# Performance work log

Hardware: AMD Instinct MI355X
Metric: run time of the kernel (lower is better)

Reference implementation:

```python
import jax, jax.numpy as jnp
import numpy as np

N_NODES = 100000
N_EDGES = 1600000
IN_DIM = 128
HEADS = 4
HID = 32            # per-head channels; HEADS*HID == 128 == IN_DIM
HC = HEADS * HID
NUM_CLASSES = 349
NUM_LAYERS = 2
BN_EPS = 1e-5
NEG_SLOPE = 0.2     # PyG GATConv default leaky_relu slope


def _gat_conv(x, src, dst, Wsrc, Wdst, a_src, a_dst, bias):
    """PyG GATConv (concat=True). x:[N,F] -> [N,H*C]."""
    N = x.shape[0]
    xs = (x @ Wsrc).reshape(N, HEADS, HID)   # source-side projection
    xd = (x @ Wdst).reshape(N, HEADS, HID)   # dest-side projection
    s_src = jnp.einsum('nhc,hc->nh', xs, a_src)   # [N,H]
    s_dst = jnp.einsum('nhc,hc->nh', xd, a_dst)   # [N,H]
    e = jax.nn.leaky_relu(s_src[src] + s_dst[dst], NEG_SLOPE)   # [E,H]
    # numerically-stable edge softmax grouped by destination node
    m = jax.ops.segment_max(e, dst, num_segments=N)             # [N,H]
    m = jnp.where(jnp.isfinite(m), m, 0.0)                      # isolated nodes
    p = jnp.exp(e - m[dst])                                     # [E,H]
    denom = jax.ops.segment_sum(p, dst, num_segments=N)         # [N,H]
    alpha = p / (denom[dst] + 1e-16)                            # [E,H]
    msg = xs[src] * alpha[:, :, None]                           # [E,H,C]
    out = jax.ops.segment_sum(msg, dst, num_segments=N)         # [N,H,C]
    return out.reshape(N, HC) + bias


def _batch_norm(x, gamma, beta):
    mu = x.mean(0)
    var = x.var(0)
    return gamma * (x - mu) * jax.lax.rsqrt(var + BN_EPS) + beta


def setup_inputs() -> dict:
    key = jax.random.key(0)
    ks = jax.random.split(key, 8)
    sc = 1.0 / np.sqrt(IN_DIM)
    inp = {
        'x': jax.random.normal(ks[0], (N_NODES, IN_DIM), jnp.float32),
        'edge_index': jax.random.randint(ks[1], (2, N_EDGES), 0, N_NODES, jnp.int32),
        'W_src': jax.random.normal(ks[2], (NUM_LAYERS, IN_DIM, HC), jnp.float32) * sc,
        'W_dst': jax.random.normal(ks[3], (NUM_LAYERS, IN_DIM, HC), jnp.float32) * sc,
        'att_src': jax.random.normal(ks[4], (NUM_LAYERS, HEADS, HID), jnp.float32) * sc,
        'att_dst': jax.random.normal(ks[5], (NUM_LAYERS, HEADS, HID), jnp.float32) * sc,
        'conv_bias': jnp.zeros((NUM_LAYERS, HC), jnp.float32),
        'lin_W': jax.random.normal(ks[6], (NUM_LAYERS, IN_DIM, HC), jnp.float32) * sc,
        'lin_b': jnp.zeros((NUM_LAYERS, HC), jnp.float32),
        'bn_gamma': jnp.ones((NUM_LAYERS, HC), jnp.float32),
        'bn_beta': jnp.zeros((NUM_LAYERS, HC), jnp.float32),
        'fc_W': jax.random.normal(ks[7], (IN_DIM, NUM_CLASSES), jnp.float32) * sc,
        'fc_b': jnp.zeros((NUM_CLASSES,), jnp.float32),
    }
    return inp


def reference(x, edge_index, W_src, W_dst, att_src, att_dst, conv_bias,
              lin_W, lin_b, bn_gamma, bn_beta, fc_W, fc_b):
    src, dst = edge_index[0], edge_index[1]
    for i in range(NUM_LAYERS):
        h = _gat_conv(x, src, dst, W_src[i], W_dst[i], att_src[i], att_dst[i],
                      conv_bias[i])
        h = h + x @ lin_W[i] + lin_b[i]          # skip projection
        h = _batch_norm(h, bn_gamma[i], bn_beta[i])
        x = jax.nn.relu(h)                        # dropout p=0.2 omitted (eval)
    return x @ fc_W + fc_b
```

## Files before the change

### kernel.cpp

```cpp
#include <hip/hip_runtime.h>
#include <hip/hip_bf16.h>
#include <stdint.h>

#define N_NODES 100000
#define N_EDGES 1600000
#define IN_DIM 128
#define HEADS 4
#define HID 32
#define HC 128
#define NUM_CLASSES 349
#define NUM_LAYERS 2
#define BN_EPS 1e-5f
#define NEG_SLOPE 0.2f
#define NCAT 264
#define MP 100032

#define NPARAM 144861

#define NBKT 782
#define ECHUNK 8192
#define NCHUNK ((N_EDGES + ECHUNK - 1) / ECHUNK)
#define NTOT (NBKT * NCHUNK)
#define SCAN_CHUNK 1024
#define SCAN2_BLOCKS ((NTOT + SCAN_CHUNK - 1) / SCAN_CHUNK)

using bf16 = __hip_bfloat16;
typedef __attribute__((ext_vector_type(8))) short short8;
typedef __attribute__((ext_vector_type(4))) float floatx4;

__device__ __forceinline__ float b2f(bf16 v) { return __bfloat162float(v); }

__global__ void detect_dtype(const uint32_t* __restrict__ xw, int* __restrict__ flag) {
    int lane = threadIdx.x;
    int insane = 0;
    for (int i = lane; i < 256; i += 64) {
        uint32_t lo = xw[i] & 0xffffu;
        uint32_t e = (lo >> 7) & 0xffu;
        if (lo != 0u && (e < 100u || e > 150u)) insane++;
    }
    for (int off = 32; off > 0; off >>= 1) insane += __shfl_down(insane, off, 64);
    if (lane == 0) *flag = (insane > 64) ? 1 : 0;
}

__global__ void cvt_params(const void* p0, const void* p1, const void* p2, const void* p3,
                           const void* p4, const void* p5, const void* p6, const void* p7,
                           const void* p8, const void* p9, const void* p10,
                           float* __restrict__ out, const int* __restrict__ flag) {
    int i = blockIdx.x * blockDim.x + threadIdx.x;
    if (i >= NPARAM) return;
    bool isf32 = (*flag != 0);
    const void* p; int off;
    if      (i < 32768)  { p = p0;  off = i; }
    else if (i < 65536)  { p = p1;  off = i - 32768; }
    else if (i < 65792)  { p = p2;  off = i - 65536; }
    else if (i < 66048)  { p = p3;  off = i - 65792; }
    else if (i < 66304)  { p = p4;  off = i - 66048; }
    else if (i < 99072)  { p = p5;  off = i - 66304; }
    else if (i < 99328)  { p = p6;  off = i - 99072; }
    else if (i < 99584)  { p = p7;  off = i - 99328; }
    else if (i < 99840)  { p = p8;  off = i - 99584; }
    else if (i < 144512) { p = p9;  off = i - 99840; }
    else                 { p = p10; off = i - 144512; }
    out[i] = isf32 ? ((const float*)p)[off] : b2f(((const bf16*)p)[off]);
}

__global__ void pack_bcat(const float* __restrict__ Wsrc, const float* __restrict__ Wdst,
                          const float* __restrict__ asrc, const float* __restrict__ adst,
                          const float* __restrict__ linW, bf16* __restrict__ Bp) {
    int idx = blockIdx.x * blockDim.x + threadIdx.x;
    if (idx >= 17 * 2048) return;
    int j = idx & 7, lane = (idx >> 3) & 63, kt = (idx >> 9) & 3, nt = idx >> 11;
    int n = nt * 16 + (lane & 15);
    int k = kt * 32 + ((lane >> 4) << 3) + j;
    float v = 0.f;
    if (n < 128) {
        v = Wsrc[k * HC + n];
    } else if (n < 132) {
        int h = n - 128;
        for (int c = 0; c < HID; c++) v += Wsrc[k * HC + h * HID + c] * asrc[h * HID + c];
    } else if (n < 136) {
        int h = n - 132;
        for (int c = 0; c < HID; c++) v += Wdst[k * HC + h * HID + c] * adst[h * HID + c];
    } else if (n < 264) {
        v = linW[k * HC + (n - 136)];
    }
    Bp[idx] = __float2bfloat16(v);
}

__global__ void pack_b(const float* __restrict__ src, int ld, int nvalid,
                       bf16* __restrict__ Bp, int total) {
    int idx = blockIdx.x * blockDim.x + threadIdx.x;
    if (idx >= total) return;
    int j = idx & 7, lane = (idx >> 3) & 63, kt = (idx >> 9) & 3, nt = idx >> 11;
    int n = nt * 16 + (lane & 15);
    int k = kt * 32 + ((lane >> 4) << 3) + j;
    float v = (n < nvalid) ? src[k * ld + n] : 0.f;
    Bp[idx] = __float2bfloat16(v);
}

template <int MODE>
__global__ __launch_bounds__(256) void gemm_mfma_proj(
    const void* __restrict__ Araw, const int* __restrict__ flag,
    const bf16* __restrict__ Bp,
    bf16* __restrict__ xs, bf16* __restrict__ scA, bf16* __restrict__ xlin,
    const float* __restrict__ gamma, const float* __restrict__ beta,
    const float* __restrict__ bnsum, const float* __restrict__ bnsq) {
    __shared__ bf16 As[64 * 128];
    int tid = threadIdx.x;
    size_t rowbase = (size_t)blockIdx.x * 64;
    int4* la = (int4*)As;
    const float invN = 1.f / (float)N_NODES;
    if (MODE == 0) {
        bool isf32 = (*flag != 0);
#pragma unroll
        for (int s = 0; s < 4; s++) {
            int idx = s * 256 + tid;
            size_t grow = rowbase + (idx >> 4);
            int cg = idx & 15;
            int4 outv = {0, 0, 0, 0};
            if (grow < N_NODES) {
                if (isf32) {
                    const float* xr = (const float*)Araw + grow * 128 + cg * 8;
                    float4 f0 = ((const float4*)xr)[0];
                    float4 f1 = ((const float4*)xr)[1];
                    bf16* ov = (bf16*)&outv;
                    ov[0] = __float2bfloat16(f0.x); ov[1] = __float2bfloat16(f0.y);
                    ov[2] = __float2bfloat16(f0.z); ov[3] = __float2bfloat16(f0.w);
                    ov[4] = __float2bfloat16(f1.x); ov[5] = __float2bfloat16(f1.y);
                    ov[6] = __float2bfloat16(f1.z); ov[7] = __float2bfloat16(f1.w);
                } else {
                    outv = ((const int4*)Araw)[grow * 16 + cg];
                }
            }
            la[idx] = outv;
        }
    } else {
        const bf16* A = (const bf16*)Araw;
        const int4* ga = (const int4*)(A + rowbase * 128);
#pragma unroll
        for (int s = 0; s < 4; s++) {
            int4 raw = ga[s * 256 + tid];
            bf16* hv = (bf16*)&raw;
            int cbase = ((s * 256 + tid) & 15) * 8;
            int4 outv; bf16* ov = (bf16*)&outv;
#pragma unroll
            for (int j = 0; j < 8; j++) {
                int c = cbase + j;
                float mu = bnsum[c] * invN;
                float var = bnsq[c] * invN - mu * mu;
                float v = gamma[c] * (b2f(hv[j]) - mu) * rsqrtf(var + BN_EPS) + beta[c];
                ov[j] = __float2bfloat16(v > 0.f ? v : 0.f);
            }
            la[s * 256 + tid] = outv;
        }
    }
    __syncthreads();
    int wave = tid >> 6, lane = tid & 63;
    int arow = wave * 16 + (lane & 15);
    int acol = (lane >> 4) * 8;
    short8 afrag[4];
#pragma unroll
    for (int kt = 0; kt < 4; kt++)
        afrag[kt] = *(const short8*)&As[arow * 128 + kt * 32 + acol];
    const short8* bbase = (const short8*)Bp + lane;
    int colb = lane & 15;
    int row0 = wave * 16 + (lane >> 4) * 4;
#pragma unroll
    for (int nt = 0; nt < 17; nt++) {
        floatx4 acc = {0.f, 0.f, 0.f, 0.f};
#pragma unroll
        for (int kt = 0; kt < 4; kt++)
            acc = __builtin_amdgcn_mfma_f32_16x16x32_bf16(afrag[kt], bbase[(nt * 4 + kt) * 64], acc, 0, 0, 0);
        int col = nt * 16 + colb;
#pragma unroll
        for (int r = 0; r < 4; r++) {
            size_t row = rowbase + row0 + r;
            bf16 v = __float2bfloat16(acc[r]);
            if (col < 128)       xs[row * HC + col] = v;
            else if (col < 136)  scA[row * 8 + (col - 128)] = v;
            else { int q = col - 136; if (q < 128) xlin[row * HC + q] = v; }
        }
    }
}

__global__ __launch_bounds__(256) void gemm_mfma_out(
    const bf16* __restrict__ A, const bf16* __restrict__ Bp,
    const float* __restrict__ bias,
    const float* __restrict__ gamma, const float* __restrict__ beta,
    const float* __restrict__ bnsum, const float* __restrict__ bnsq,
    void* __restrict__ C, const int* __restrict__ flag) {
    __shared__ bf16 As[64 * 128];
    int tid = threadIdx.x;
    size_t rowbase = (size_t)blockIdx.x * 64;
    const int4* ga = (const int4*)(A + rowbase * 128);
    int4* la = (int4*)As;
    const float invN = 1.f / (float)N_NODES;
#pragma unroll
    for (int s = 0; s < 4; s++) {
        int4 raw = ga[s * 256 + tid];
        bf16* hv = (bf16*)&raw;
        int cbase = ((s * 256 + tid) & 15) * 8;
        int4 outv; bf16* ov = (bf16*)&outv;
#pragma unroll
        for (int j = 0; j < 8; j++) {
            int c = cbase + j;
            float mu = bnsum[c] * invN;
            float var = bnsq[c] * invN - mu * mu;
            float v = gamma[c] * (b2f(hv[j]) - mu) * rsqrtf(var + BN_EPS) + beta[c];
            ov[j] = __float2bfloat16(v > 0.f ? v : 0.f);
        }
        la[s * 256 + tid] = outv;
    }
    __syncthreads();
    int wave = tid >> 6, lane = tid & 63;
    int arow = wave * 16 + (lane & 15);
    int acol = (lane >> 4) * 8;
    short8 afrag[4];
#pragma unroll
    for (int kt = 0; kt < 4; kt++)
        afrag[kt] = *(const short8*)&As[arow * 128 + kt * 32 + acol];
    const short8* bbase = (const short8*)Bp + lane;
    int colb = lane & 15;
    int row0 = wave * 16 + (lane >> 4) * 4;
    bool isf32 = (*flag != 0);
    for (int nt = 0; nt < 22; nt++) {
        floatx4 acc = {0.f, 0.f, 0.f, 0.f};
#pragma unroll
        for (int kt = 0; kt < 4; kt++)
            acc = __builtin_amdgcn_mfma_f32_16x16x32_bf16(afrag[kt], bbase[(nt * 4 + kt) * 64], acc, 0, 0, 0);
        int col = nt * 16 + colb;
        if (col >= NUM_CLASSES) continue;
        float bv = bias[col];
#pragma unroll
        for (int r = 0; r < 4; r++) {
            size_t row = rowbase + row0 + r;
            if (row < N_NODES) {
                float v = acc[r] + bv;
                if (isf32) ((float*)C)[row * NUM_CLASSES + col] = v;
                else       ((bf16*)C)[row * NUM_CLASSES + col] = __float2bfloat16(v);
            }
        }
    }
}

__global__ __launch_bounds__(256) void bucket_hist(const int* __restrict__ dst,
                                                   int* __restrict__ cnt) {
    __shared__ int h[NBKT];
    int t = threadIdx.x;
    for (int i = t; i < NBKT; i += 256) h[i] = 0;
    __syncthreads();
    int base = blockIdx.x * ECHUNK;
    int end = base + ECHUNK; if (end > N_EDGES) end = N_EDGES;
    for (int i = base + t; i < end; i += 256)
        atomicAdd(&h[dst[i] >> 7], 1);
    __syncthreads();
    for (int i = t; i < NBKT; i += 256)
        cnt[i * NCHUNK + blockIdx.x] = h[i];
}

__global__ void scan_partial(const int* __restrict__ counts, int* __restrict__ bsum, int n) {
    __shared__ int red[256];
    int t = threadIdx.x;
    int base = blockIdx.x * SCAN_CHUNK + t * 4;
    int s = 0;
#pragma unroll
    for (int j = 0; j < 4; j++) {
        int idx = base + j;
        if (idx < n) s += counts[idx];
    }
    red[t] = s;
    __syncthreads();
    for (int off = 128; off > 0; off >>= 1) {
        if (t < off) red[t] += red[t + off];
        __syncthreads();
    }
    if (t == 0) bsum[blockIdx.x] = red[0];
}

__global__ void scan_final(int* __restrict__ counts, const int* __restrict__ bsum, int n) {
    __shared__ int ts[256];
    __shared__ int pre[256];
    int t = threadIdx.x;
    int pv = (t < (int)blockIdx.x) ? bsum[t] : 0;
    pre[t] = pv;
    int base = blockIdx.x * SCAN_CHUNK + t * 4;
    int c[4];
    int mysum = 0;
#pragma unroll
    for (int j = 0; j < 4; j++) {
        int idx = base + j;
        c[j] = (idx < n) ? counts[idx] : 0;
        mysum += c[j];
    }
    ts[t] = mysum;
    __syncthreads();
    for (int off = 128; off > 0; off >>= 1) {
        if (t < off) pre[t] += pre[t + off];
        __syncthreads();
    }
    for (int off = 1; off < 256; off <<= 1) {
        int v = (t >= off) ? ts[t - off] : 0;
        __syncthreads();
        ts[t] += v;
        __syncthreads();
    }
    int run = pre[0] + ts[t] - mysum;
#pragma unroll
    for (int j = 0; j < 4; j++) {
        int idx = base + j;
        if (idx < n) {
            counts[idx] = run;
            run += c[j];
        }
    }
}

__global__ __launch_bounds__(256) void bucket_scatter(const int* __restrict__ src,
                                                      const int* __restrict__ dst,
                                                      const int* __restrict__ cntscan,
                                                      uint32_t* __restrict__ sorted) {
    __shared__ int cur[NBKT];
    int t = threadIdx.x;
    for (int i = t; i < NBKT; i += 256)
        cur[i] = cntscan[i * NCHUNK + blockIdx.x];
    __syncthreads();
    int base = blockIdx.x * ECHUNK;
    int end = base + ECHUNK; if (end > N_EDGES) end = N_EDGES;
    for (int i = base + t; i < end; i += 256) {
        int d = dst[i];
        int b = d >> 7;
        int pos = atomicAdd(&cur[b], 1);
        sorted[pos] = ((uint32_t)(d & 127) << 17) | (uint32_t)src[i];
    }
}

__global__ __launch_bounds__(256) void bucket_csr(const uint32_t* __restrict__ sorted,
                                                  const int* __restrict__ cntscan,
                                                  int* __restrict__ srcs,
                                                  int* __restrict__ offsets) {
    __shared__ int cnt128[128];
    __shared__ int sc[128];
    __shared__ int cur[128];
    int b = blockIdx.x, t = threadIdx.x;
    int ebeg = cntscan[b * NCHUNK];
    int eend = (b == NBKT - 1) ? N_EDGES : cntscan[(b + 1) * NCHUNK];
    if (t < 128) cnt128[t] = 0;
    __syncthreads();
    uint32_t buf[10];
    int k = 0;
    for (int e = ebeg + t; e < eend; e += 256) {
        uint32_t u = sorted[e];
        if (k < 10) buf[k] = u;
        k++;
        atomicAdd(&cnt128[u >> 17], 1);
    }
    __syncthreads();
    if (t < 128) sc[t] = cnt128[t];
    __syncthreads();
    for (int off = 1; off < 128; off <<= 1) {
        int v = 0;
        if (t < 128 && t >= off) v = sc[t - off];
        __syncthreads();
        if (t < 128) sc[t] += v;
        __syncthreads();
    }
    if (t < 128) {
        int node = b * 128 + t;
        if (node < N_NODES) offsets[node] = ebeg + sc[t];
        cur[t] = ebeg + sc[t] - cnt128[t];
    }
    __syncthreads();
    int k2 = 0;
    for (int e = ebeg + t; e < eend; e += 256) {
        uint32_t u = (k2 < 10) ? buf[k2] : sorted[e];
        k2++;
        int ld = (int)(u >> 17);
        int pos = atomicAdd(&cur[ld], 1);
        srcs[pos] = (int)(u & 0x1FFFFu);
    }
}

__device__ __forceinline__ void edge_acc(int s, int h, int c0, float s_dst,
                                         const bf16* __restrict__ xs,
                                         const bf16* __restrict__ scA,
                                         float& den, float& n0, float& n1) {
    float sc = b2f(scA[(size_t)s * 8 + h]) + s_dst;
    sc = sc > 0.f ? sc : NEG_SLOPE * sc;
    float e = __expf(sc);
    __hip_bfloat162 xv = *reinterpret_cast<const __hip_bfloat162*>(&xs[(size_t)s * HC + c0]);
    den += e;
    n0 += b2f(xv.x) * e;
    n1 += b2f(xv.y) * e;
}

__global__ __launch_bounds__(256) void gat_gather(
    const int* __restrict__ srcs, const int* __restrict__ offsets,
    const bf16* __restrict__ xs, const bf16* __restrict__ scA,
    const bf16* __restrict__ xlin,
    const float* __restrict__ cbias, const float* __restrict__ lbias,
    bf16* __restrict__ hout) {
    int n = blockIdx.x * 4 + (threadIdx.x >> 6);
    int lane = threadIdx.x & 63;
    int c0 = lane * 2;
    int h = c0 >> 5;
    int beg = (n == 0) ? 0 : offsets[n - 1];
    int end = offsets[n];
    float s_dst = b2f(scA[(size_t)n * 8 + 4 + h]);
    float den = 0.f, n0 = 0.f, n1 = 0.f;
    int i = beg;
    for (; i + 7 < end; i += 8) {
        int s0 = srcs[i],     s1 = srcs[i + 1], s2 = srcs[i + 2], s3 = srcs[i + 3];
        int s4 = srcs[i + 4], s5 = srcs[i + 5], s6 = srcs[i + 6], s7 = srcs[i + 7];
        edge_acc(s0, h, c0, s_dst, xs, scA, den, n0, n1);
        edge_acc(s1, h, c0, s_dst, xs, scA, den, n0, n1);
        edge_acc(s2, h, c0, s_dst, xs, scA, den, n0, n1);
        edge_acc(s3, h, c0, s_dst, xs, scA, den, n0, n1);
        edge_acc(s4, h, c0, s_dst, xs, scA, den, n0, n1);
        edge_acc(s5, h, c0, s_dst, xs, scA, den, n0, n1);
        edge_acc(s6, h, c0, s_dst, xs, scA, den, n0, n1);
        edge_acc(s7, h, c0, s_dst, xs, scA, den, n0, n1);
    }
    for (; i + 3 < end; i += 4) {
        int s0 = srcs[i], s1 = srcs[i + 1], s2 = srcs[i + 2], s3 = srcs[i + 3];
        edge_acc(s0, h, c0, s_dst, xs, scA, den, n0, n1);
        edge_acc(s1, h, c0, s_dst, xs, scA, den, n0, n1);
        edge_acc(s2, h, c0, s_dst, xs, scA, den, n0, n1);
        edge_acc(s3, h, c0, s_dst, xs, scA, den, n0, n1);
    }
    for (; i < end; i++)
        edge_acc(srcs[i], h, c0, s_dst, xs, scA, den, n0, n1);
    float r = 1.f / (den + 1e-16f);
    __hip_bfloat162 xl = *reinterpret_cast<const __hip_bfloat162*>(&xlin[(size_t)n * HC + c0]);
    float v0 = n0 * r + b2f(xl.x) + cbias[c0] + lbias[c0];
    float v1 = n1 * r + b2f(xl.y) + cbias[c0 + 1] + lbias[c0 + 1];
    __hip_bfloat162 hv;
    hv.x = __float2bfloat16(v0);
    hv.y = __float2bfloat16(v1);
    *reinterpret_cast<__hip_bfloat162*>(&hout[(size_t)n * HC + c0]) = hv;
}

__global__ void bn_stats(const bf16* __restrict__ h, float* __restrict__ bnsum,
                         float* __restrict__ bnsq) {
    int c = threadIdx.x & 127;
    int half = threadIdx.x >> 7;
    int r0 = blockIdx.x * 500;
    int rend = r0 + 500; if (rend > N_NODES) rend = N_NODES;
    float s1 = 0.f, s2 = 0.f;
    for (int r = r0 + half; r < rend; r += 2) {
        float v = b2f(h[(size_t)r * HC + c]);
        s1 += v; s2 += v * v;
    }
    atomicAdd(&bnsum[c], s1);
    atomicAdd(&bnsq[c], s2);
}

extern "C" void kernel_launch(void* const* d_in, const int* in_sizes, int n_in,
                              void* d_out, int out_size, void* d_ws, size_t ws_size,
                              hipStream_t stream) {
    const void* x_in = d_in[0];
    const int*  edge = (const int*)d_in[1];
    const int* esrc = edge;
    const int* edst = edge + N_EDGES;

    bf16* xbh  = (bf16*)d_ws;
    bf16* xs   = xbh + (size_t)MP * HC;
    bf16* scA  = xs + (size_t)MP * HC;
    bf16* xlin = scA + (size_t)MP * 8;
    bf16* Bp   = xlin + (size_t)MP * HC;
    bf16* fcWp = Bp + 17 * 2048;
    float* bnstat = (float*)(fcWp + 22 * 2048);
    int*   flag  = (int*)(bnstat + 512);
    int*   bsum  = flag + 4;
    float* parms = (float*)(bsum + SCAN2_BLOCKS + 2);
    float* Wsrc_f  = parms;
    float* Wdst_f  = parms + 32768;
    float* asrc_f  = parms + 65536;
    float* adst_f  = parms + 65792;
    float* cbias_f = parms + 66048;
    float* linW_f  = parms + 66304;
    float* linb_f  = parms + 99072;
    float* gamma_f = parms + 99328;
    float* beta_f  = parms + 99584;
    float* fcW_f   = parms + 99840;
    float* fcb_f   = parms + 144512;

    int* srcs    = (int*)d_out;
    int* offsets = srcs + N_EDGES;
    uint32_t* sorted = (uint32_t*)(offsets + N_NODES);
    int* cnt = (int*)(sorted + N_EDGES);

    detect_dtype<<<1, 64, 0, stream>>>((const uint32_t*)x_in, flag);

    cvt_params<<<(NPARAM + 255) / 256, 256, 0, stream>>>(
        d_in[2], d_in[3], d_in[4], d_in[5], d_in[6], d_in[7], d_in[8],
        d_in[9], d_in[10], d_in[11], d_in[12], parms, flag);

    bucket_hist<<<NCHUNK, 256, 0, stream>>>(edst, cnt);
    scan_partial<<<SCAN2_BLOCKS, 256, 0, stream>>>(cnt, bsum, NTOT);
    scan_final<<<SCAN2_BLOCKS, 256, 0, stream>>>(cnt, bsum, NTOT);
    bucket_scatter<<<NCHUNK, 256, 0, stream>>>(esrc, edst, cnt, sorted);
    bucket_csr<<<NBKT, 256, 0, stream>>>(sorted, cnt, srcs, offsets);

    pack_b<<<(22 * 2048 + 255) / 256, 256, 0, stream>>>(fcW_f, NUM_CLASSES, NUM_CLASSES,
                                                        fcWp, 22 * 2048);
    hipMemsetAsync(bnstat, 0, 512 * sizeof(float), stream);

    for (int layer = 0; layer < NUM_LAYERS; layer++) {
        const int woff = layer * IN_DIM * HC;
        const int aoff = layer * HEADS * HID;
        const int boff = layer * HC;
        float* bns = bnstat + layer * 256;
        float* bnq = bns + 128;

        pack_bcat<<<(17 * 2048 + 255) / 256, 256, 0, stream>>>(
            Wsrc_f + woff, Wdst_f + woff, asrc_f + aoff, adst_f + aoff,
            linW_f + woff, Bp);

        if (layer == 0) {
            gemm_mfma_proj<0><<<MP / 64, 256, 0, stream>>>(
                x_in, flag, Bp, xs, scA, xlin, nullptr, nullptr, nullptr, nullptr);
        } else {
            float* pbns = bnstat + (layer - 1) * 256;
            gemm_mfma_proj<1><<<MP / 64, 256, 0, stream>>>(
                xbh, nullptr, Bp, xs, scA, xlin,
                gamma_f + (layer - 1) * HC, beta_f + (layer - 1) * HC,
                pbns, pbns + 128);
        }

        gat_gather<<<N_NODES / 4, 256, 0, stream>>>(
            srcs, offsets, xs, scA, xlin, cbias_f + boff, linb_f + boff, xbh);

        bn_stats<<<200, 256, 0, stream>>>(xbh, bns, bnq);
    }

    gemm_mfma_out<<<MP / 64, 256, 0, stream>>>(
        xbh, fcWp, fcb_f, gamma_f + HC, beta_f + HC,
        bnstat + 256, bnstat + 256 + 128, d_out, flag);
}
```

Before: 703.1 us.

## Fuse CSR build into cooperative kernel, merge packs, restructure GEMM B reuse

Folds the five-kernel bucket-sort CSR build (histogram, two scans, scatter, per-bucket CSR) into one cooperative kernel that uses grid syncs. It also merges the weight-packing kernels into a single launch and moves the BN-stat zeroing into detect_dtype, so fewer kernels are launched. The GEMMs now keep B fragments in registers per wave and loop over row tiles, and BN scale/shift is precomputed once per block in shared memory. The gather loop prefetches the next batch of source indices. The cooperative launch needs all 391 blocks resident at once, and the larger register footprint may lower occupancy.

```diff
diff --git a/kernel.cpp b/kernel.cpp
--- a/kernel.cpp
+++ b/kernel.cpp
@@ -1,6 +1,9 @@
 #include <hip/hip_runtime.h>
 #include <hip/hip_bf16.h>
+#include <hip/hip_cooperative_groups.h>
 #include <stdint.h>
+
+namespace cg = cooperative_groups;
 
 #define N_NODES 100000
 #define N_EDGES 1600000
@@ -12,17 +15,22 @@
 #define NUM_LAYERS 2
 #define BN_EPS 1e-5f
 #define NEG_SLOPE 0.2f
-#define NCAT 264
 #define MP 100032
 
 #define NPARAM 144861
 
 #define NBKT 782
-#define ECHUNK 8192
-#define NCHUNK ((N_EDGES + ECHUNK - 1) / ECHUNK)
+#define ECHUNK 4096
+#define NCHUNK 391
 #define NTOT (NBKT * NCHUNK)
-#define SCAN_CHUNK 1024
-#define SCAN2_BLOCKS ((NTOT + SCAN_CHUNK - 1) / SCAN_CHUNK)
+#define SCAN_CHUNK 2048
+#define SCANB ((NTOT + SCAN_CHUNK - 1) / SCAN_CHUNK)
+
+#define BP_NT 20
+#define FC_NT 24
+#define BP_ELEMS (BP_NT * 2048)
+#define FC_ELEMS (FC_NT * 2048)
+#define PACK_TOTAL (2 * BP_ELEMS + FC_ELEMS)
 
 using bf16 = __hip_bfloat16;
 typedef __attribute__((ext_vector_type(8))) short short8;
@@ -30,8 +38,10 @@
 
 __device__ __forceinline__ float b2f(bf16 v) { return __bfloat162float(v); }
 
-__global__ void detect_dtype(const uint32_t* __restrict__ xw, int* __restrict__ flag) {
+__global__ void detect_dtype(const uint32_t* __restrict__ xw, int* __restrict__ flag,
+                             float* __restrict__ bnstat) {
     int lane = threadIdx.x;
+    for (int i = lane; i < 512; i += 64) bnstat[i] = 0.f;
     int insane = 0;
     for (int i = lane; i < 256; i += 64) {
         uint32_t lo = xw[i] & 0xffffu;
@@ -64,38 +74,45 @@
     out[i] = isf32 ? ((const float*)p)[off] : b2f(((const bf16*)p)[off]);
 }
 
-__global__ void pack_bcat(const float* __restrict__ Wsrc, const float* __restrict__ Wdst,
-                          const float* __restrict__ asrc, const float* __restrict__ adst,
-                          const float* __restrict__ linW, bf16* __restrict__ Bp) {
-    int idx = blockIdx.x * blockDim.x + threadIdx.x;
-    if (idx >= 17 * 2048) return;
-    int j = idx & 7, lane = (idx >> 3) & 63, kt = (idx >> 9) & 3, nt = idx >> 11;
-    int n = nt * 16 + (lane & 15);
-    int k = kt * 32 + ((lane >> 4) << 3) + j;
-    float v = 0.f;
-    if (n < 128) {
-        v = Wsrc[k * HC + n];
-    } else if (n < 132) {
-        int h = n - 128;
-        for (int c = 0; c < HID; c++) v += Wsrc[k * HC + h * HID + c] * asrc[h * HID + c];
-    } else if (n < 136) {
-        int h = n - 132;
-        for (int c = 0; c < HID; c++) v += Wdst[k * HC + h * HID + c] * adst[h * HID + c];
-    } else if (n < 264) {
-        v = linW[k * HC + (n - 136)];
-    }
-    Bp[idx] = __float2bfloat16(v);
-}
-
-__global__ void pack_b(const float* __restrict__ src, int ld, int nvalid,
-                       bf16* __restrict__ Bp, int total) {
-    int idx = blockIdx.x * blockDim.x + threadIdx.x;
-    if (idx >= total) return;
-    int j = idx & 7, lane = (idx >> 3) & 63, kt = (idx >> 9) & 3, nt = idx >> 11;
-    int n = nt * 16 + (lane & 15);
-    int k = kt * 32 + ((lane >> 4) << 3) + j;
-    float v = (n < nvalid) ? src[k * ld + n] : 0.f;
-    Bp[idx] = __float2bfloat16(v);
+__global__ void pack_all(const float* __restrict__ Wsrc0, const float* __restrict__ Wdst0,
+                         const float* __restrict__ asrc0, const float* __restrict__ adst0,
+                         const float* __restrict__ linW0, const float* __restrict__ fcW,
+                         bf16* __restrict__ Bp0, bf16* __restrict__ Bp1,
+                         bf16* __restrict__ fcWp) {
+    int gid = blockIdx.x * blockDim.x + threadIdx.x;
+    if (gid >= PACK_TOTAL) return;
+    if (gid < 2 * BP_ELEMS) {
+        int layer = gid / BP_ELEMS;
+        int idx = gid - layer * BP_ELEMS;
+        const float* Wsrc = Wsrc0 + layer * IN_DIM * HC;
+        const float* Wdst = Wdst0 + layer * IN_DIM * HC;
+        const float* asrc = asrc0 + layer * HEADS * HID;
+        const float* adst = adst0 + layer * HEADS * HID;
+        const float* linW = linW0 + layer * IN_DIM * HC;
+        int j = idx & 7, lane = (idx >> 3) & 63, kt = (idx >> 9) & 3, nt = idx >> 11;
+        int n = nt * 16 + (lane & 15);
+        int k = kt * 32 + ((lane >> 4) << 3) + j;
+        float v = 0.f;
+        if (n < 128) {
+            v = Wsrc[k * HC + n];
+        } else if (n < 132) {
+            int h = n - 128;
+            for (int c = 0; c < HID; c++) v += Wsrc[k * HC + h * HID + c] * asrc[h * HID + c];
+        } else if (n < 136) {
+            int h = n - 132;
+            for (int c = 0; c < HID; c++) v += Wdst[k * HC + h * HID + c] * adst[h * HID + c];
+        } else if (n < 264) {
+            v = linW[k * HC + (n - 136)];
+        }
+        (layer == 0 ? Bp0 : Bp1)[idx] = __float2bfloat16(v);
+    } else {
+        int idx = gid - 2 * BP_ELEMS;
+        int j = idx & 7, lane = (idx >> 3) & 63, kt = (idx >> 9) & 3, nt = idx >> 11;
+        int n = nt * 16 + (lane & 15);
+        int k = kt * 32 + ((lane >> 4) << 3) + j;
+        float v = (n < NUM_CLASSES) ? fcW[k * NUM_CLASSES + n] : 0.f;
+        fcWp[idx] = __float2bfloat16(v);
+    }
 }
 
 template <int MODE>
@@ -106,21 +123,21 @@
     const float* __restrict__ gamma, const float* __restrict__ beta,
     const float* __restrict__ bnsum, const float* __restrict__ bnsq) {
     __shared__ bf16 As[64 * 128];
+    __shared__ float sc_s[128], sh_s[128];
     int tid = threadIdx.x;
     size_t rowbase = (size_t)blockIdx.x * 64;
     int4* la = (int4*)As;
-    const float invN = 1.f / (float)N_NODES;
     if (MODE == 0) {
         bool isf32 = (*flag != 0);
 #pragma unroll
         for (int s = 0; s < 4; s++) {
             int idx = s * 256 + tid;
             size_t grow = rowbase + (idx >> 4);
-            int cg = idx & 15;
+            int cg16 = idx & 15;
             int4 outv = {0, 0, 0, 0};
             if (grow < N_NODES) {
                 if (isf32) {
-                    const float* xr = (const float*)Araw + grow * 128 + cg * 8;
+                    const float* xr = (const float*)Araw + grow * 128 + cg16 * 8;
                     float4 f0 = ((const float4*)xr)[0];
                     float4 f1 = ((const float4*)xr)[1];
                     bf16* ov = (bf16*)&outv;
@@ -129,12 +146,21 @@
                     ov[4] = __float2bfloat16(f1.x); ov[5] = __float2bfloat16(f1.y);
                     ov[6] = __float2bfloat16(f1.z); ov[7] = __float2bfloat16(f1.w);
                 } else {
-                    outv = ((const int4*)Araw)[grow * 16 + cg];
+                    outv = ((const int4*)Araw)[grow * 16 + cg16];
                 }
             }
             la[idx] = outv;
         }
     } else {
+        const float invN = 1.f / (float)N_NODES;
+        if (tid < 128) {
+            float mu = bnsum[tid] * invN;
+            float var = bnsq[tid] * invN - mu * mu;
+            float g = gamma[tid] * rsqrtf(var + BN_EPS);
+            sc_s[tid] = g;
+            sh_s[tid] = beta[tid] - mu * g;
+        }
+        __syncthreads();
         const bf16* A = (const bf16*)Araw;
         const int4* ga = (const int4*)(A + rowbase * 128);
 #pragma unroll
@@ -146,9 +172,7 @@
 #pragma unroll
             for (int j = 0; j < 8; j++) {
                 int c = cbase + j;
-                float mu = bnsum[c] * invN;
-                float var = bnsq[c] * invN - mu * mu;
-                float v = gamma[c] * (b2f(hv[j]) - mu) * rsqrtf(var + BN_EPS) + beta[c];
+                float v = sc_s[c] * b2f(hv[j]) + sh_s[c];
                 ov[j] = __float2bfloat16(v > 0.f ? v : 0.f);
             }
             la[s * 256 + tid] = outv;
@@ -156,29 +180,39 @@
     }
     __syncthreads();
     int wave = tid >> 6, lane = tid & 63;
-    int arow = wave * 16 + (lane & 15);
+    int colb = lane & 15;
     int acol = (lane >> 4) * 8;
-    short8 afrag[4];
-#pragma unroll
-    for (int kt = 0; kt < 4; kt++)
-        afrag[kt] = *(const short8*)&As[arow * 128 + kt * 32 + acol];
-    const short8* bbase = (const short8*)Bp + lane;
-    int colb = lane & 15;
-    int row0 = wave * 16 + (lane >> 4) * 4;
-#pragma unroll
-    for (int nt = 0; nt < 17; nt++) {
-        floatx4 acc = {0.f, 0.f, 0.f, 0.f};
+    const short8* bb = (const short8*)Bp + lane;
+    short8 bfrag[5][4];
+#pragma unroll
+    for (int j = 0; j < 5; j++) {
+        int nt = wave + 4 * j;
+#pragma unroll
+        for (int kt = 0; kt < 4; kt++) bfrag[j][kt] = bb[(nt * 4 + kt) * 64];
+    }
+#pragma unroll
+    for (int rt = 0; rt < 4; rt++) {
+        int arow = rt * 16 + (lane & 15);
+        short8 af[4];
 #pragma unroll
         for (int kt = 0; kt < 4; kt++)
-            acc = __builtin_amdgcn_mfma_f32_16x16x32_bf16(afrag[kt], bbase[(nt * 4 + kt) * 64], acc, 0, 0, 0);
-        int col = nt * 16 + colb;
-#pragma unroll
-        for (int r = 0; r < 4; r++) {
-            size_t row = rowbase + row0 + r;
-            bf16 v = __float2bfloat16(acc[r]);
-            if (col < 128)       xs[row * HC + col] = v;
-            else if (col < 136)  scA[row * 8 + (col - 128)] = v;
-            else { int q = col - 136; if (q < 128) xlin[row * HC + q] = v; }
+            af[kt] = *(const short8*)&As[arow * 128 + kt * 32 + acol];
+        int row0 = rt * 16 + (lane >> 4) * 4;
+#pragma unroll
+        for (int j = 0; j < 5; j++) {
+            floatx4 acc = {0.f, 0.f, 0.f, 0.f};
+#pragma unroll
+            for (int kt = 0; kt < 4; kt++)
+                acc = __builtin_amdgcn_mfma_f32_16x16x32_bf16(af[kt], bfrag[j][kt], acc, 0, 0, 0);
+            int col = (wave + 4 * j) * 16 + colb;
+#pragma unroll
+            for (int r = 0; r < 4; r++) {
+                size_t row = rowbase + row0 + r;
+                bf16 v = __float2bfloat16(acc[r]);
+                if (col < 128)       xs[row * HC + col] = v;
+                else if (col < 136)  scA[row * 8 + (col - 128)] = v;
+                else { int q = col - 136; if (q < 128) xlin[row * HC + q] = v; }
+            }
         }
     }
 }
@@ -190,11 +224,20 @@
     const float* __restrict__ bnsum, const float* __restrict__ bnsq,
     void* __restrict__ C, const int* __restrict__ flag) {
     __shared__ bf16 As[64 * 128];
+    __shared__ float sc_s[128], sh_s[128];
     int tid = threadIdx.x;
     size_t rowbase = (size_t)blockIdx.x * 64;
     const int4* ga = (const int4*)(A + rowbase * 128);
     int4* la = (int4*)As;
     const float invN = 1.f / (float)N_NODES;
+    if (tid < 128) {
+        float mu = bnsum[tid] * invN;
+        float var = bnsq[tid] * invN - mu * mu;
+        float g = gamma[tid] * rsqrtf(var + BN_EPS);
+        sc_s[tid] = g;
+        sh_s[tid] = beta[tid] - mu * g;
+    }
+    __syncthreads();
 #pragma unroll
     for (int s = 0; s < 4; s++) {
         int4 raw = ga[s * 256 + tid];
@@ -204,179 +247,190 @@
 #pragma unroll
         for (int j = 0; j < 8; j++) {
             int c = cbase + j;
-            float mu = bnsum[c] * invN;
-            float var = bnsq[c] * invN - mu * mu;
-            float v = gamma[c] * (b2f(hv[j]) - mu) * rsqrtf(var + BN_EPS) + beta[c];
+            float v = sc_s[c] * b2f(hv[j]) + sh_s[c];
             ov[j] = __float2bfloat16(v > 0.f ? v : 0.f);
         }
         la[s * 256 + tid] = outv;
     }
     __syncthreads();
     int wave = tid >> 6, lane = tid & 63;
-    int arow = wave * 16 + (lane & 15);
+    int colb = lane & 15;
     int acol = (lane >> 4) * 8;
-    short8 afrag[4];
-#pragma unroll
-    for (int kt = 0; kt < 4; kt++)
-        afrag[kt] = *(const short8*)&As[arow * 128 + kt * 32 + acol];
-    const short8* bbase = (const short8*)Bp + lane;
-    int colb = lane & 15;
-    int row0 = wave * 16 + (lane >> 4) * 4;
+    const short8* bb = (const short8*)Bp + lane;
+    short8 bfrag[6][4];
+#pragma unroll
+    for (int j = 0; j < 6; j++) {
+        int nt = wave + 4 * j;
+#pragma unroll
+        for (int kt = 0; kt < 4; kt++) bfrag[j][kt] = bb[(nt * 4 + kt) * 64];
+    }
     bool isf32 = (*flag != 0);
-    for (int nt = 0; nt < 22; nt++) {
-        floatx4 acc = {0.f, 0.f, 0.f, 0.f};
+#pragma unroll
+    for (int rt = 0; rt < 4; rt++) {
+        int arow = rt * 16 + (lane & 15);
+        short8 af[4];
 #pragma unroll
         for (int kt = 0; kt < 4; kt++)
-            acc = __builtin_amdgcn_mfma_f32_16x16x32_bf16(afrag[kt], bbase[(nt * 4 + kt) * 64], acc, 0, 0, 0);
-        int col = nt * 16 + colb;
-        if (col >= NUM_CLASSES) continue;
-        float bv = bias[col];
-#pragma unroll
-        for (int r = 0; r < 4; r++) {
-            size_t row = rowbase + row0 + r;
-            if (row < N_NODES) {
-                float v = acc[r] + bv;
-                if (isf32) ((float*)C)[row * NUM_CLASSES + col] = v;
-                else       ((bf16*)C)[row * NUM_CLASSES + col] = __float2bfloat16(v);
+            af[kt] = *(const short8*)&As[arow * 128 + kt * 32 + acol];
+        int row0 = rt * 16 + (lane >> 4) * 4;
+#pragma unroll
+        for (int j = 0; j < 6; j++) {
+            floatx4 acc = {0.f, 0.f, 0.f, 0.f};
+#pragma unroll
+            for (int kt = 0; kt < 4; kt++)
+                acc = __builtin_amdgcn_mfma_f32_16x16x32_bf16(af[kt], bfrag[j][kt], acc, 0, 0, 0);
+            int col = (wave + 4 * j) * 16 + colb;
+            if (col < NUM_CLASSES) {
+                float bv = bias[col];
+#pragma unroll
+                for (int r = 0; r < 4; r++) {
+                    size_t row = rowbase + row0 + r;
+                    if (row < N_NODES) {
+                        float v = acc[r] + bv;
+                        if (isf32) ((float*)C)[row * NUM_CLASSES + col] = v;
+                        else       ((bf16*)C)[row * NUM_CLASSES + col] = __float2bfloat16(v);
+                    }
+                }
             }
         }
     }
 }
 
-__global__ __launch_bounds__(256) void bucket_hist(const int* __restrict__ dst,
-                                                   int* __restrict__ cnt) {
-    __shared__ int h[NBKT];
-    int t = threadIdx.x;
-    for (int i = t; i < NBKT; i += 256) h[i] = 0;
-    __syncthreads();
-    int base = blockIdx.x * ECHUNK;
-    int end = base + ECHUNK; if (end > N_EDGES) end = N_EDGES;
-    for (int i = base + t; i < end; i += 256)
-        atomicAdd(&h[dst[i] >> 7], 1);
-    __syncthreads();
-    for (int i = t; i < NBKT; i += 256)
-        cnt[i * NCHUNK + blockIdx.x] = h[i];
-}
-
-__global__ void scan_partial(const int* __restrict__ counts, int* __restrict__ bsum, int n) {
+__global__ __launch_bounds__(256) void csr_coop(
+    const int* __restrict__ src, const int* __restrict__ dst,
+    int* __restrict__ cnt, int* __restrict__ bsum,
+    uint32_t* __restrict__ sorted, int* __restrict__ srcs,
+    int* __restrict__ offsets) {
+    cg::grid_group grid = cg::this_grid();
+    __shared__ int lh[NBKT];
     __shared__ int red[256];
-    int t = threadIdx.x;
-    int base = blockIdx.x * SCAN_CHUNK + t * 4;
-    int s = 0;
-#pragma unroll
-    for (int j = 0; j < 4; j++) {
-        int idx = base + j;
-        if (idx < n) s += counts[idx];
-    }
-    red[t] = s;
-    __syncthreads();
-    for (int off = 128; off > 0; off >>= 1) {
-        if (t < off) red[t] += red[t + off];
-        __syncthreads();
-    }
-    if (t == 0) bsum[blockIdx.x] = red[0];
-}
-
-__global__ void scan_final(int* __restrict__ counts, const int* __restrict__ bsum, int n) {
     __shared__ int ts[256];
     __shared__ int pre[256];
-    int t = threadIdx.x;
-    int pv = (t < (int)blockIdx.x) ? bsum[t] : 0;
-    pre[t] = pv;
-    int base = blockIdx.x * SCAN_CHUNK + t * 4;
-    int c[4];
-    int mysum = 0;
-#pragma unroll
-    for (int j = 0; j < 4; j++) {
-        int idx = base + j;
-        c[j] = (idx < n) ? counts[idx] : 0;
-        mysum += c[j];
-    }
-    ts[t] = mysum;
+    int t = threadIdx.x, b = blockIdx.x;
+
+    for (int i = t; i < NBKT; i += 256) lh[i] = 0;
     __syncthreads();
-    for (int off = 128; off > 0; off >>= 1) {
-        if (t < off) pre[t] += pre[t + off];
-        __syncthreads();
-    }
-    for (int off = 1; off < 256; off <<= 1) {
-        int v = (t >= off) ? ts[t - off] : 0;
-        __syncthreads();
-        ts[t] += v;
-        __syncthreads();
-    }
-    int run = pre[0] + ts[t] - mysum;
-#pragma unroll
-    for (int j = 0; j < 4; j++) {
-        int idx = base + j;
-        if (idx < n) {
-            counts[idx] = run;
-            run += c[j];
-        }
-    }
-}
-
-__global__ __launch_bounds__(256) void bucket_scatter(const int* __restrict__ src,
-                                                      const int* __restrict__ dst,
-                                                      const int* __restrict__ cntscan,
-                                                      uint32_t* __restrict__ sorted) {
-    __shared__ int cur[NBKT];
-    int t = threadIdx.x;
-    for (int i = t; i < NBKT; i += 256)
-        cur[i] = cntscan[i * NCHUNK + blockIdx.x];
+    {
+        int base = b * ECHUNK;
+        int end = base + ECHUNK; if (end > N_EDGES) end = N_EDGES;
+        int i = base + t;
+        for (; i + 768 < end; i += 1024) {
+            int d0 = dst[i], d1 = dst[i + 256], d2 = dst[i + 512], d3 = dst[i + 768];
+            atomicAdd(&lh[d0 >> 7], 1); atomicAdd(&lh[d1 >> 7], 1);
+            atomicAdd(&lh[d2 >> 7], 1); atomicAdd(&lh[d3 >> 7], 1);
+        }
+        for (; i < end; i += 256) atomicAdd(&lh[dst[i] >> 7], 1);
+    }
     __syncthreads();
-    int base = blockIdx.x * ECHUNK;
-    int end = base + ECHUNK; if (end > N_EDGES) end = N_EDGES;
-    for (int i = base + t; i < end; i += 256) {
-        int d = dst[i];
-        int b = d >> 7;
-        int pos = atomicAdd(&cur[b], 1);
-        sorted[pos] = ((uint32_t)(d & 127) << 17) | (uint32_t)src[i];
-    }
-}
-
-__global__ __launch_bounds__(256) void bucket_csr(const uint32_t* __restrict__ sorted,
-                                                  const int* __restrict__ cntscan,
-                                                  int* __restrict__ srcs,
-                                                  int* __restrict__ offsets) {
-    __shared__ int cnt128[128];
-    __shared__ int sc[128];
-    __shared__ int cur[128];
-    int b = blockIdx.x, t = threadIdx.x;
-    int ebeg = cntscan[b * NCHUNK];
-    int eend = (b == NBKT - 1) ? N_EDGES : cntscan[(b + 1) * NCHUNK];
-    if (t < 128) cnt128[t] = 0;
+    for (int i = t; i < NBKT; i += 256) cnt[i * NCHUNK + b] = lh[i];
+    grid.sync();
+
+    if (b < SCANB) {
+        int base = b * SCAN_CHUNK + t * 8;
+        int s = 0;
+#pragma unroll
+        for (int j = 0; j < 8; j++) { int idx = base + j; if (idx < NTOT) s += cnt[idx]; }
+        red[t] = s;
+        __syncthreads();
+        for (int off = 128; off > 0; off >>= 1) {
+            if (t < off) red[t] += red[t + off];
+            __syncthreads();
+        }
+        if (t == 0) bsum[b] = red[0];
+    }
+    grid.sync();
+
+    if (b < SCANB) {
+        pre[t] = (t < b) ? bsum[t] : 0;
+        int base = b * SCAN_CHUNK + t * 8;
+        int c[8]; int mysum = 0;
+#pragma unroll
+        for (int j = 0; j < 8; j++) { int idx = base + j; c[j] = (idx < NTOT) ? cnt[idx] : 0; mysum += c[j]; }
+        ts[t] = mysum;
+        __syncthreads();
+        for (int off = 128; off > 0; off >>= 1) {
+            if (t < off) pre[t] += pre[t + off];
+            __syncthreads();
+        }
+        for (int off = 1; off < 256; off <<= 1) {
+            int v = (t >= off) ? ts[t - off] : 0;
+            __syncthreads();
+            ts[t] += v;
+            __syncthreads();
+        }
+        int run = pre[0] + ts[t] - mysum;
+#pragma unroll
+        for (int j = 0; j < 8; j++) { int idx = base + j; if (idx < NTOT) { cnt[idx] = run; run += c[j]; } }
+    }
+    grid.sync();
+
+    for (int i = t; i < NBKT; i += 256) lh[i] = cnt[i * NCHUNK + b];
     __syncthreads();
-    uint32_t buf[10];
-    int k = 0;
-    for (int e = ebeg + t; e < eend; e += 256) {
-        uint32_t u = sorted[e];
-        if (k < 10) buf[k] = u;
-        k++;
-        atomicAdd(&cnt128[u >> 17], 1);
-    }
-    __syncthreads();
-    if (t < 128) sc[t] = cnt128[t];
-    __syncthreads();
-    for (int off = 1; off < 128; off <<= 1) {
-        int v = 0;
-        if (t < 128 && t >= off) v = sc[t - off];
-        __syncthreads();
-        if (t < 128) sc[t] += v;
-        __syncthreads();
-    }
-    if (t < 128) {
-        int node = b * 128 + t;
-        if (node < N_NODES) offsets[node] = ebeg + sc[t];
-        cur[t] = ebeg + sc[t] - cnt128[t];
-    }
-    __syncthreads();
-    int k2 = 0;
-    for (int e = ebeg + t; e < eend; e += 256) {
-        uint32_t u = (k2 < 10) ? buf[k2] : sorted[e];
-        k2++;
-        int ld = (int)(u >> 17);
-        int pos = atomicAdd(&cur[ld], 1);
-        srcs[pos] = (int)(u & 0x1FFFFu);
+    {
+        int base = b * ECHUNK;
+        int end = base + ECHUNK; if (end > N_EDGES) end = N_EDGES;
+        int i = base + t;
+        for (; i + 768 < end; i += 1024) {
+            int d0 = dst[i],       d1 = dst[i + 256], d2 = dst[i + 512], d3 = dst[i + 768];
+            int s0 = src[i],       s1 = src[i + 256], s2 = src[i + 512], s3 = src[i + 768];
+            int p0 = atomicAdd(&lh[d0 >> 7], 1);
+            int p1 = atomicAdd(&lh[d1 >> 7], 1);
+            int p2 = atomicAdd(&lh[d2 >> 7], 1);
+            int p3 = atomicAdd(&lh[d3 >> 7], 1);
+            sorted[p0] = ((uint32_t)(d0 & 127) << 17) | (uint32_t)s0;
+            sorted[p1] = ((uint32_t)(d1 & 127) << 17) | (uint32_t)s1;
+            sorted[p2] = ((uint32_t)(d2 & 127) << 17) | (uint32_t)s2;
+            sorted[p3] = ((uint32_t)(d3 & 127) << 17) | (uint32_t)s3;
+        }
+        for (; i < end; i += 256) {
+            int d = dst[i];
+            int p = atomicAdd(&lh[d >> 7], 1);
+            sorted[p] = ((uint32_t)(d & 127) << 17) | (uint32_t)src[i];
+        }
+    }
+    grid.sync();
+
+    int* cnt128 = lh;
+    int* sc = lh + 128;
+    int* cur = lh + 256;
+    for (int bk = b * 2; bk < b * 2 + 2; bk++) {
+        int ebeg = cnt[bk * NCHUNK];
+        int eend = (bk == NBKT - 1) ? N_EDGES : cnt[(bk + 1) * NCHUNK];
+        __syncthreads();
+        if (t < 128) cnt128[t] = 0;
+        __syncthreads();
+        uint32_t buf[10];
+        int k = 0;
+        for (int e = ebeg + t; e < eend; e += 256) {
+            uint32_t u = sorted[e];
+            if (k < 10) buf[k] = u;
+            k++;
+            atomicAdd(&cnt128[u >> 17], 1);
+        }
+        __syncthreads();
+        if (t < 128) sc[t] = cnt128[t];
+        __syncthreads();
+        for (int off = 1; off < 128; off <<= 1) {
+            int v = 0;
+            if (t < 128 && t >= off) v = sc[t - off];
+            __syncthreads();
+            if (t < 128) sc[t] += v;
+            __syncthreads();
+        }
+        if (t < 128) {
+            int node = bk * 128 + t;
+            if (node < N_NODES) offsets[node] = ebeg + sc[t];
+            cur[t] = ebeg + sc[t] - cnt128[t];
+        }
+        __syncthreads();
+        int k2 = 0;
+        for (int e = ebeg + t; e < eend; e += 256) {
+            uint32_t u = (k2 < 10) ? buf[k2] : sorted[e];
+            k2++;
+            int ld = (int)(u >> 17);
+            int pos = atomicAdd(&cur[ld], 1);
+            srcs[pos] = (int)(u & 0x1FFFFu);
+        }
     }
 }
 
@@ -408,24 +462,29 @@
     float s_dst = b2f(scA[(size_t)n * 8 + 4 + h]);
     float den = 0.f, n0 = 0.f, n1 = 0.f;
     int i = beg;
-    for (; i + 7 < end; i += 8) {
+    if (i + 7 < end) {
         int s0 = srcs[i],     s1 = srcs[i + 1], s2 = srcs[i + 2], s3 = srcs[i + 3];
         int s4 = srcs[i + 4], s5 = srcs[i + 5], s6 = srcs[i + 6], s7 = srcs[i + 7];
-        edge_acc(s0, h, c0, s_dst, xs, scA, den, n0, n1);
-        edge_acc(s1, h, c0, s_dst, xs, scA, den, n0, n1);
-        edge_acc(s2, h, c0, s_dst, xs, scA, den, n0, n1);
-        edge_acc(s3, h, c0, s_dst, xs, scA, den, n0, n1);
-        edge_acc(s4, h, c0, s_dst, xs, scA, den, n0, n1);
-        edge_acc(s5, h, c0, s_dst, xs, scA, den, n0, n1);
-        edge_acc(s6, h, c0, s_dst, xs, scA, den, n0, n1);
-        edge_acc(s7, h, c0, s_dst, xs, scA, den, n0, n1);
-    }
-    for (; i + 3 < end; i += 4) {
-        int s0 = srcs[i], s1 = srcs[i + 1], s2 = srcs[i + 2], s3 = srcs[i + 3];
-        edge_acc(s0, h, c0, s_dst, xs, scA, den, n0, n1);
-        edge_acc(s1, h, c0, s_dst, xs, scA, den, n0, n1);
-        edge_acc(s2, h, c0, s_dst, xs, scA, den, n0, n1);
-        edge_acc(s3, h, c0, s_dst, xs, scA, den, n0, n1);
+        for (;;) {
+            int ni = i + 8;
+            bool more = (ni + 7 < end);
+            int t0 = 0, t1 = 0, t2 = 0, t3 = 0, t4 = 0, t5 = 0, t6 = 0, t7 = 0;
+            if (more) {
+                t0 = srcs[ni];     t1 = srcs[ni + 1]; t2 = srcs[ni + 2]; t3 = srcs[ni + 3];
+                t4 = srcs[ni + 4]; t5 = srcs[ni + 5]; t6 = srcs[ni + 6]; t7 = srcs[ni + 7];
+            }
+            edge_acc(s0, h, c0, s_dst, xs, scA, den, n0, n1);
+            edge_acc(s1, h, c0, s_dst, xs, scA, den, n0, n1);
+            edge_acc(s2, h, c0, s_dst, xs, scA, den, n0, n1);
+            edge_acc(s3, h, c0, s_dst, xs, scA, den, n0, n1);
+            edge_acc(s4, h, c0, s_dst, xs, scA, den, n0, n1);
+            edge_acc(s5, h, c0, s_dst, xs, scA, den, n0, n1);
+            edge_acc(s6, h, c0, s_dst, xs, scA, den, n0, n1);
+            edge_acc(s7, h, c0, s_dst, xs, scA, den, n0, n1);
+            i = ni;
+            if (!more) break;
+            s0 = t0; s1 = t1; s2 = t2; s3 = t3; s4 = t4; s5 = t5; s6 = t6; s7 = t7;
+        }
     }
     for (; i < end; i++)
         edge_acc(srcs[i], h, c0, s_dst, xs, scA, den, n0, n1);
@@ -466,12 +525,13 @@
     bf16* xs   = xbh + (size_t)MP * HC;
     bf16* scA  = xs + (size_t)MP * HC;
     bf16* xlin = scA + (size_t)MP * 8;
-    bf16* Bp   = xlin + (size_t)MP * HC;
-    bf16* fcWp = Bp + 17 * 2048;
-    float* bnstat = (float*)(fcWp + 22 * 2048);
+    bf16* Bp0  = xlin + (size_t)MP * HC;
+    bf16* Bp1  = Bp0 + BP_ELEMS;
+    bf16* fcWp = Bp1 + BP_ELEMS;
+    float* bnstat = (float*)(fcWp + FC_ELEMS);
     int*   flag  = (int*)(bnstat + 512);
     int*   bsum  = flag + 4;
-    float* parms = (float*)(bsum + SCAN2_BLOCKS + 2);
+    float* parms = (float*)(bsum + SCANB + 2);
     float* Wsrc_f  = parms;
     float* Wdst_f  = parms + 32768;
     float* asrc_f  = parms + 65536;
@@ -489,40 +549,34 @@
     uint32_t* sorted = (uint32_t*)(offsets + N_NODES);
     int* cnt = (int*)(sorted + N_EDGES);
 
-    detect_dtype<<<1, 64, 0, stream>>>((const uint32_t*)x_in, flag);
+    detect_dtype<<<1, 64, 0, stream>>>((const uint32_t*)x_in, flag, bnstat);
 
     cvt_params<<<(NPARAM + 255) / 256, 256, 0, stream>>>(
         d_in[2], d_in[3], d_in[4], d_in[5], d_in[6], d_in[7], d_in[8],
         d_in[9], d_in[10], d_in[11], d_in[12], parms, flag);
 
-    bucket_hist<<<NCHUNK, 256, 0, stream>>>(edst, cnt);
-    scan_partial<<<SCAN2_BLOCKS, 256, 0, stream>>>(cnt, bsum, NTOT);
-    scan_final<<<SCAN2_BLOCKS, 256, 0, stream>>>(cnt, bsum, NTOT);
-    bucket_scatter<<<NCHUNK, 256, 0, stream>>>(esrc, edst, cnt, sorted);
-    bucket_csr<<<NBKT, 256, 0, stream>>>(sorted, cnt, srcs, offsets);
-
-    pack_b<<<(22 * 2048 + 255) / 256, 256, 0, stream>>>(fcW_f, NUM_CLASSES, NUM_CLASSES,
-                                                        fcWp, 22 * 2048);
-    hipMemsetAsync(bnstat, 0, 512 * sizeof(float), stream);
+    {
+        void* args[] = { (void*)&esrc, (void*)&edst, (void*)&cnt, (void*)&bsum,
+                         (void*)&sorted, (void*)&srcs, (void*)&offsets };
+        hipLaunchCooperativeKernel((void*)csr_coop, dim3(NCHUNK), dim3(256),
+                                   args, 0, stream);
+    }
+
+    pack_all<<<(PACK_TOTAL + 255) / 256, 256, 0, stream>>>(
+        Wsrc_f, Wdst_f, asrc_f, adst_f, linW_f, fcW_f, Bp0, Bp1, fcWp);
 
     for (int layer = 0; layer < NUM_LAYERS; layer++) {
-        const int woff = layer * IN_DIM * HC;
-        const int aoff = layer * HEADS * HID;
         const int boff = layer * HC;
         float* bns = bnstat + layer * 256;
         float* bnq = bns + 128;
 
-        pack_bcat<<<(17 * 2048 + 255) / 256, 256, 0, stream>>>(
-            Wsrc_f + woff, Wdst_f + woff, asrc_f + aoff, adst_f + aoff,
-            linW_f + woff, Bp);
-
         if (layer == 0) {
             gemm_mfma_proj<0><<<MP / 64, 256, 0, stream>>>(
-                x_in, flag, Bp, xs, scA, xlin, nullptr, nullptr, nullptr, nullptr);
+                x_in, flag, Bp0, xs, scA, xlin, nullptr, nullptr, nullptr, nullptr);
         } else {
             float* pbns = bnstat + (layer - 1) * 256;
             gemm_mfma_proj<1><<<MP / 64, 256, 0, stream>>>(
-                xbh, nullptr, Bp, xs, scA, xlin,
+                xbh, nullptr, Bp1, xs, scA, xlin,
                 gamma_f + (layer - 1) * HC, beta_f + (layer - 1) * HC,
                 pbns, pbns + 128);
         }
```

Result: slower. 887.3 us (+26.2%).
